# Performance work log

Measured on AMD Instinct MI355X. Metric: run time of the kernel, lower is better.

Reference implementation:

```python
import jax, jax.numpy as jnp
import numpy as np

HEADS = 16
NEG_INF = np.float32(-2**32 + 1)  # matches TF code's padding value


def setup_inputs() -> dict:
    key = jax.random.key(0)
    ks = jax.random.split(key, 11)
    B, S, D = 2, 2048, 1024
    mk = lambda k, shape: jax.random.normal(k, shape, dtype=jnp.float32)
    return {
        "query": mk(ks[0], (B, S, D)),
        "key":   mk(ks[1], (B, S, D)),
        "value": mk(ks[2], (B, S, D)),
        "Wq": mk(ks[3], (D, D)) * (1.0 / np.sqrt(D)), "bq": jnp.zeros((D,), jnp.float32),
        "Wk": mk(ks[4], (D, D)) * (1.0 / np.sqrt(D)), "bk": jnp.zeros((D,), jnp.float32),
        "Wv": mk(ks[5], (D, D)) * (1.0 / np.sqrt(D)), "bv": jnp.zeros((D,), jnp.float32),
        "Wo": mk(ks[6], (D, D)) * (1.0 / np.sqrt(D)), "bo": jnp.zeros((D,), jnp.float32),
    }


def reference(query, key, value, Wq, bq, Wk, bk, Wv, bv, Wo, bo):
    B, S, D = query.shape
    H = HEADS
    dh = D // H
    # QKV projections with relu (as in the original Dense(activation=relu))
    q = jax.nn.relu(query @ Wq + bq).reshape(B, S, H, dh)
    k = jax.nn.relu(key   @ Wk + bk).reshape(B, S, H, dh)
    v = jax.nn.relu(value @ Wv + bv).reshape(B, S, H, dh)
    # scaled dot-product attention; scale = sqrt(per-head key dim)
    scores = jnp.einsum("bqhd,bkhd->bhqk", q, k) / jnp.sqrt(jnp.float32(dh))
    # causal mask (masked=True path): zeros above the diagonal -> NEG_INF
    causal = jnp.tril(jnp.ones((S, S), dtype=jnp.float32))  # [S,S]
    scores = jnp.where(causal == 0, NEG_INF, scores)
    attn = jax.nn.softmax(scores, axis=-1)  # [B,H,S,S]
    out = jnp.einsum("bhqk,bkhd->bqhd", attn, v).reshape(B, S, D)
    return jax.nn.relu(out @ Wo + bo)
```

## Files before the change

### kernel.cpp

```cpp
#include <hip/hip_runtime.h>
#include <hip/hip_bf16.h>

using bf16 = __hip_bfloat16;
typedef __attribute__((ext_vector_type(8))) short bf16x8;
typedef __attribute__((ext_vector_type(4))) float f32x4;

#define DEV __device__ __forceinline__

DEV void gload_lds16(const void* g, void* l) {
  __builtin_amdgcn_global_load_lds((const __attribute__((address_space(1))) void*)g,
                                   (__attribute__((address_space(3))) void*)l, 16, 0, 0);
}

DEV unsigned pk2(float lo, float hi) {
  union { bf16 h[2]; unsigned u; } z;
  z.h[0] = __float2bfloat16(lo);
  z.h[1] = __float2bfloat16(hi);
  return z.u;
}

struct PrepArgs {
  const float* x[3]; bf16* y[3];
  const float* W[4]; bf16* WT[4];
};

__global__ __launch_bounds__(256) void prep_kernel(PrepArgs a) {
  __shared__ float tile[32][33];
  const int b = blockIdx.x;
  if (b < 6144) {
    const int which = b >> 11, blk = b & 2047;
    const int i = blk * 256 + threadIdx.x;
    const float4* xv = (const float4*)a.x[which];
    float4 p = xv[i * 2];
    float4 q = xv[i * 2 + 1];
    union { bf16 h[8]; uint4 v; } u;
    u.h[0] = __float2bfloat16(p.x); u.h[1] = __float2bfloat16(p.y);
    u.h[2] = __float2bfloat16(p.z); u.h[3] = __float2bfloat16(p.w);
    u.h[4] = __float2bfloat16(q.x); u.h[5] = __float2bfloat16(q.y);
    u.h[6] = __float2bfloat16(q.z); u.h[7] = __float2bfloat16(q.w);
    *(uint4*)&a.y[which][(size_t)i * 8] = u.v;
  } else {
    const int w = (b - 6144) >> 10, blk = (b - 6144) & 1023;
    const float* W = a.W[w];
    bf16* WT = a.WT[w];
    const int tx = threadIdx.x & 31, ty = threadIdx.x >> 5;
    const int n0 = (blk & 31) * 32, k0 = (blk >> 5) * 32;
#pragma unroll
    for (int i = ty; i < 32; i += 8)
      tile[i][tx] = W[(size_t)(k0 + i) * 1024 + n0 + tx];
    __syncthreads();
#pragma unroll
    for (int i = ty; i < 32; i += 8)
      WT[(size_t)(n0 + i) * 1024 + k0 + tx] = __float2bfloat16(tile[tx][i]);
  }
}

__global__ __launch_bounds__(256) void vtrans_kernel(const bf16* __restrict__ v,
                                                     bf16* __restrict__ VT) {
  __shared__ bf16 tile[64 * 64];
  const int t = threadIdx.x;
  const int bh = blockIdx.y, b = bh >> 4, h = bh & 15;
  const int s0 = blockIdx.x * 64;
  const int r0 = t >> 3, c8 = t & 7;
#pragma unroll
  for (int it = 0; it < 2; ++it) {
    int r = it * 32 + r0;
    uint4 d = *(const uint4*)&v[(size_t)(b * 2048 + s0 + r) * 1024 + h * 64 + c8 * 8];
    *(uint4*)&tile[r * 64 + ((c8 ^ (r >> 3)) * 8)] = d;
  }
  __syncthreads();
#pragma unroll
  for (int it = 0; it < 2; ++it) {
    int d = it * 32 + r0;
    int sc = c8 * 8;
    union { bf16 h[8]; uint4 v4; } u;
#pragma unroll
    for (int j = 0; j < 8; ++j) {
      int row = sc + j;
      u.h[j] = tile[row * 64 + (((d >> 3) ^ (row >> 3)) * 8) + (d & 7)];
    }
    *(uint4*)&VT[((size_t)bh * 64 + d) * 2048 + s0 + sc] = u.v4;
  }
}

template <typename OutT>
DEV void gemm128_core(const bf16* __restrict__ A, const bf16* __restrict__ BT,
                      const float* __restrict__ bias, OutT* __restrict__ out) {
  constexpr int K = 1024, N = 1024;
  __shared__ bf16 ldsA[2][128 * 32];
  __shared__ bf16 ldsB[2][128 * 32];
  const int t = threadIdx.x;
  const int lane = t & 63, wid = t >> 6;
  const int wr = wid >> 1, wc = wid & 1;
  const int fr = lane & 15, fko = (lane >> 4) * 8;
  const size_t mBase = (size_t)blockIdx.y * 128;
  const size_t nBase = (size_t)blockIdx.x * 128;

  const int srow = t >> 2;
  const int scol = (t & 3) * 8;
  const bf16* gA = A + (mBase + srow) * K + scol;
  const bf16* gB = BT + (nBase + srow) * K + scol;
  const int ldst = wid * 512;

  f32x4 acc[4][4];
#pragma unroll
  for (int i = 0; i < 4; ++i)
#pragma unroll
    for (int j = 0; j < 4; ++j) acc[i][j] = (f32x4){0.f, 0.f, 0.f, 0.f};

  gload_lds16(gA, &ldsA[0][ldst]);
  gload_lds16(gA + 64 * K, &ldsA[0][ldst + 2048]);
  gload_lds16(gB, &ldsB[0][ldst]);
  gload_lds16(gB + 64 * K, &ldsB[0][ldst + 2048]);
  __syncthreads();

  int buf = 0;
  for (int k0 = 0; k0 < K; k0 += 32) {
    if (k0 + 32 < K) {
      const int kn = k0 + 32;
      gload_lds16(gA + kn, &ldsA[buf ^ 1][ldst]);
      gload_lds16(gA + 64 * K + kn, &ldsA[buf ^ 1][ldst + 2048]);
      gload_lds16(gB + kn, &ldsB[buf ^ 1][ldst]);
      gload_lds16(gB + 64 * K + kn, &ldsB[buf ^ 1][ldst + 2048]);
    }
    bf16x8 aF[4], bF[4];
#pragma unroll
    for (int i = 0; i < 4; ++i)
      aF[i] = *(const bf16x8*)&ldsA[buf][(wr * 64 + i * 16 + fr) * 32 + fko];
#pragma unroll
    for (int j = 0; j < 4; ++j)
      bF[j] = *(const bf16x8*)&ldsB[buf][(wc * 64 + j * 16 + fr) * 32 + fko];
#pragma unroll
    for (int i = 0; i < 4; ++i)
#pragma unroll
      for (int j = 0; j < 4; ++j)
        acc[i][j] = __builtin_amdgcn_mfma_f32_16x16x32_bf16(aF[i], bF[j], acc[i][j], 0, 0, 0);
    __syncthreads();
    buf ^= 1;
  }

  const int orow = (int)mBase + wr * 64 + (lane >> 4) * 4;
  const int ocol = (int)nBase + wc * 64 + fr;
#pragma unroll
  for (int j = 0; j < 4; ++j) {
    const float bj = bias[ocol + j * 16];
#pragma unroll
    for (int i = 0; i < 4; ++i)
#pragma unroll
      for (int r = 0; r < 4; ++r) {
        float v = fmaxf(acc[i][j][r] + bj, 0.f);
        size_t idx = (size_t)(orow + i * 16 + r) * N + (ocol + j * 16);
        if constexpr (sizeof(OutT) == 2) out[idx] = __float2bfloat16(v);
        else out[idx] = v;
      }
  }
}

struct QKVArgs {
  const bf16* A[3];
  const bf16* BT[3];
  const float* bias[3];
  bf16* out[3];
};

__global__ __launch_bounds__(256) void gemm_qkv_kernel(QKVArgs args) {
  const int z = blockIdx.z;
  gemm128_core<bf16>(args.A[z], args.BT[z], args.bias[z], args.out[z]);
}

__global__ __launch_bounds__(256) void gemm_out_kernel(const bf16* __restrict__ A,
                                                       const bf16* __restrict__ BT,
                                                       const float* __restrict__ bias,
                                                       float* __restrict__ out) {
  gemm128_core<float>(A, BT, bias, out);
}

__global__ __launch_bounds__(256, 4) void attn_kernel(const bf16* __restrict__ Qb,
                                                      const bf16* __restrict__ Kb,
                                                      const bf16* __restrict__ VTb,
                                                      bf16* __restrict__ Ob) {
  constexpr int Dm = 1024, S = 2048;
  __shared__ bf16 ldsKV[16384];
  const int t = threadIdx.x, l = t & 63, wid = t >> 6;

  const int lin = blockIdx.y * 16 + blockIdx.x;
  const int swz = (lin & 7) * 64 + (lin >> 3);
  const int bh = swz >> 4, pairp = swz & 15;
  const int b = bh >> 4, h = bh & 15;
  const int q4 = l & 15, fg = l >> 4;
  const bf16* Qg = Qb + (size_t)b * S * Dm + h * 64;
  const bf16* Kg = Kb + (size_t)b * S * Dm + h * 64;
  const bf16* VTg = VTb + (size_t)bh * 64 * S;

  const int srow = l >> 3;
  const int schunk = (l & 7) ^ srow;
  const bf16* kSrc = Kg + (size_t)(wid * 16 + srow) * Dm + schunk * 8;
  const bf16* vSrc = VTg + (size_t)(wid * 16 + srow) * S + schunk * 8;
  bf16* kDst = ldsKV + wid * 1024;
  bf16* vDst = ldsKV + 8192 + wid * 1024;

  const int idx0 = ((q4 + ((l & 16) ? 32 : 0)) << 2);
  const int idx1 = idx0 + 64;

#pragma unroll 1
  for (int ph = 0; ph < 2; ++ph) {
    const int qt = ph ? (31 - pairp) : pairp;
    const int qb = qt * 64;
    const int qw = qb + wid * 16;

    bf16x8 qF[2];
#pragma unroll
    for (int kd = 0; kd < 2; ++kd)
      qF[kd] = *(const bf16x8*)&Qg[(size_t)(qw + q4) * Dm + kd * 32 + fg * 8];

    f32x4 oacc[4];
#pragma unroll
    for (int n = 0; n < 4; ++n) oacc[n] = (f32x4){0.f, 0.f, 0.f, 0.f};
    float mrow = -3.0e38f, lsum = 0.f;

    const int nTiles = qt + 1;

    gload_lds16(kSrc, kDst);
    gload_lds16(kSrc + 8 * Dm, kDst + 512);
    gload_lds16(vSrc, vDst);
    gload_lds16(vSrc + 8 * S, vDst + 512);
    __syncthreads();

    int buf = 0;
    for (int tile = 0; tile < nTiles; ++tile) {
      const int kvb = tile * 64;
      if (tile + 1 < nTiles) {
        const int nb = kvb + 64;
        gload_lds16(kSrc + (size_t)nb * Dm, kDst + (buf ^ 1) * 4096);
        gload_lds16(kSrc + (size_t)(nb + 8) * Dm, kDst + (buf ^ 1) * 4096 + 512);
        gload_lds16(vSrc + nb, vDst + (buf ^ 1) * 4096);
        gload_lds16(vSrc + nb + 8 * S, vDst + (buf ^ 1) * 4096 + 512);
      }
      const bf16* kb = ldsKV + buf * 4096;
      const bf16* vb = ldsKV + 8192 + buf * 4096;

      f32x4 sT[4];
#pragma unroll
      for (int n = 0; n < 4; ++n) sT[n] = (f32x4){0.f, 0.f, 0.f, 0.f};
      __builtin_amdgcn_s_setprio(1);
#pragma unroll
      for (int n = 0; n < 4; ++n) {
#pragma unroll
        for (int kd = 0; kd < 2; ++kd) {
          bf16x8 kf = *(const bf16x8*)&kb[(n * 16 + q4) * 64 + (((kd * 4 + fg) ^ (q4 & 7)) * 8)];
          sT[n] = __builtin_amdgcn_mfma_f32_16x16x32_bf16(kf, qF[kd], sT[n], 0, 0, 0);
        }
      }
      __builtin_amdgcn_s_setprio(0);
      const bool needmask = (tile == nTiles - 1);
      const int qrow = qw + q4;
#pragma unroll
      for (int n = 0; n < 4; ++n)
#pragma unroll
        for (int r = 0; r < 4; ++r) {
          float vv = sT[n][r] * 0.125f;
          if (needmask) {
            int kv = kvb + n * 16 + fg * 4 + r;
            if (kv > qrow) vv = -1e30f;
          }
          sT[n][r] = vv;
        }
      float tmax = -3.0e38f;
#pragma unroll
      for (int n = 0; n < 4; ++n)
        tmax = fmaxf(tmax, fmaxf(fmaxf(sT[n][0], sT[n][1]), fmaxf(sT[n][2], sT[n][3])));
      tmax = fmaxf(tmax, __shfl_xor(tmax, 16, 64));
      tmax = fmaxf(tmax, __shfl_xor(tmax, 32, 64));
      const float mnew = fmaxf(mrow, tmax);
      const float corr = __expf(mrow - mnew);
      mrow = mnew;
      float rs = 0.f;
#pragma unroll
      for (int n = 0; n < 4; ++n)
#pragma unroll
        for (int r = 0; r < 4; ++r) {
          float p = __expf(sT[n][r] - mnew);
          sT[n][r] = p;
          rs += p;
        }
      rs += __shfl_xor(rs, 16, 64);
      rs += __shfl_xor(rs, 32, 64);
      lsum = lsum * corr + rs;
#pragma unroll
      for (int n = 0; n < 4; ++n)
#pragma unroll
        for (int r = 0; r < 4; ++r) oacc[n][r] *= corr;

#pragma unroll
      for (int ks = 0; ks < 2; ++ks) {
        const unsigned X0 = pk2(sT[2 * ks][0], sT[2 * ks][1]);
        const unsigned X1 = pk2(sT[2 * ks][2], sT[2 * ks][3]);
        const unsigned Y0 = pk2(sT[2 * ks + 1][0], sT[2 * ks + 1][1]);
        const unsigned Y1 = pk2(sT[2 * ks + 1][2], sT[2 * ks + 1][3]);
        union { int u[4]; bf16x8 v; } bfr;
        {
          int zx = __builtin_amdgcn_ds_bpermute(idx0, (int)X0);
          int zy = __builtin_amdgcn_ds_bpermute(idx0, (int)Y0);
          bfr.u[0] = (l & 32) ? zy : zx;
          zx = __builtin_amdgcn_ds_bpermute(idx0, (int)X1);
          zy = __builtin_amdgcn_ds_bpermute(idx0, (int)Y1);
          bfr.u[1] = (l & 32) ? zy : zx;
          zx = __builtin_amdgcn_ds_bpermute(idx1, (int)X0);
          zy = __builtin_amdgcn_ds_bpermute(idx1, (int)Y0);
          bfr.u[2] = (l & 32) ? zy : zx;
          zx = __builtin_amdgcn_ds_bpermute(idx1, (int)X1);
          zy = __builtin_amdgcn_ds_bpermute(idx1, (int)Y1);
          bfr.u[3] = (l & 32) ? zy : zx;
        }
        __builtin_amdgcn_s_setprio(1);
#pragma unroll
        for (int dblk = 0; dblk < 4; ++dblk) {
          bf16x8 vf = *(const bf16x8*)&vb[(dblk * 16 + q4) * 64 + (((ks * 4 + fg) ^ (q4 & 7)) * 8)];
          oacc[dblk] = __builtin_amdgcn_mfma_f32_16x16x32_bf16(vf, bfr.v, oacc[dblk], 0, 0, 0);
        }
        __builtin_amdgcn_s_setprio(0);
      }
      __syncthreads();
      buf ^= 1;
    }

    bf16* ldsT = ldsKV + wid * 1152;
    const float inv = 1.f / lsum;
#pragma unroll
    for (int dblk = 0; dblk < 4; ++dblk)
#pragma unroll
      for (int r = 0; r < 4; ++r) {
        int d = dblk * 16 + fg * 4 + r;
        ldsT[q4 * 72 + d] = __float2bfloat16(oacc[dblk][r] * inv);
      }
    asm volatile("s_waitcnt lgkmcnt(0)" ::: "memory");
    __builtin_amdgcn_sched_barrier(0);
    const int rq = l >> 2, dq = (l & 3) * 16;
#pragma unroll
    for (int i = 0; i < 2; ++i) {
      uint4 w = *(const uint4*)&ldsT[rq * 72 + dq + 8 * i];
      *(uint4*)&Ob[((size_t)b * S + qw + rq) * Dm + h * 64 + dq + 8 * i] = w;
    }
    __syncthreads();
  }
}

extern "C" void kernel_launch(void* const* d_in, const int* in_sizes, int n_in,
                              void* d_out, int out_size, void* d_ws, size_t ws_size,
                              hipStream_t stream) {
  const float* query = (const float*)d_in[0];
  const float* key   = (const float*)d_in[1];
  const float* value = (const float*)d_in[2];
  const float* Wq = (const float*)d_in[3]; const float* bq = (const float*)d_in[4];
  const float* Wk = (const float*)d_in[5]; const float* bk = (const float*)d_in[6];
  const float* Wv = (const float*)d_in[7]; const float* bv = (const float*)d_in[8];
  const float* Wo = (const float*)d_in[9]; const float* bo = (const float*)d_in[10];
  float* out = (float*)d_out;

  char* ws = (char*)d_ws;
  const size_t MB = 1024 * 1024;
  bf16* xq  = (bf16*)(ws + 0 * MB);
  bf16* xk  = (bf16*)(ws + 8 * MB);
  bf16* xv  = (bf16*)(ws + 16 * MB);
  bf16* qp  = (bf16*)(ws + 24 * MB);
  bf16* kp  = (bf16*)(ws + 32 * MB);
  bf16* vp  = (bf16*)(ws + 40 * MB);
  bf16* WqT = (bf16*)(ws + 48 * MB);
  bf16* WkT = (bf16*)(ws + 50 * MB);
  bf16* WvT = (bf16*)(ws + 52 * MB);
  bf16* WoT = (bf16*)(ws + 54 * MB);
  bf16* VT   = xq;
  bf16* attn = xk;

  PrepArgs pa;
  pa.x[0] = query; pa.x[1] = key; pa.x[2] = value;
  pa.y[0] = xq; pa.y[1] = xk; pa.y[2] = xv;
  pa.W[0] = Wq; pa.W[1] = Wk; pa.W[2] = Wv; pa.W[3] = Wo;
  pa.WT[0] = WqT; pa.WT[1] = WkT; pa.WT[2] = WvT; pa.WT[3] = WoT;
  prep_kernel<<<10240, 256, 0, stream>>>(pa);

  QKVArgs qa;
  qa.A[0] = xq;  qa.A[1] = xk;  qa.A[2] = xv;
  qa.BT[0] = WqT; qa.BT[1] = WkT; qa.BT[2] = WvT;
  qa.bias[0] = bq; qa.bias[1] = bk; qa.bias[2] = bv;
  qa.out[0] = qp; qa.out[1] = kp; qa.out[2] = vp;
  gemm_qkv_kernel<<<dim3(8, 32, 3), 256, 0, stream>>>(qa);

  vtrans_kernel<<<dim3(32, 32), 256, 0, stream>>>(vp, VT);
  attn_kernel<<<dim3(16, 32), 256, 0, stream>>>(qp, kp, VT, attn);
  gemm_out_kernel<<<dim3(8, 32), 256, 0, stream>>>(attn, WoT, bo, out);
}
```

Measured before the change: 233.7 us.

## Use exp2 softmax with lazy rescale and smaller output GEMM tiles

The attention softmax now folds log2(e) into the score scale and uses the hardware exp2 instruction. The running-max rescale of the accumulators is skipped unless some row's max grows by more than 8 (in log2 units). This cuts exp and multiply work per tile, at the cost of intermediate values that can reach up to 2^8 before bf16 packing. Separately, the output projection GEMM uses 64-row tiles with twice as many blocks to fill the GPU better, and both GEMM kernels get launch_bounds occupancy hints.

```diff
diff --git a/kernel.cpp b/kernel.cpp
--- a/kernel.cpp
+++ b/kernel.cpp
@@ -6,6 +6,8 @@
 typedef __attribute__((ext_vector_type(4))) float f32x4;
 
 #define DEV __device__ __forceinline__
+
+DEV float exp2fast(float x) { return __builtin_amdgcn_exp2f(x); }
 
 DEV void gload_lds16(const void* g, void* l) {
   __builtin_amdgcn_global_load_lds((const __attribute__((address_space(1))) void*)g,
@@ -83,17 +85,18 @@
   }
 }
 
-template <typename OutT>
-DEV void gemm128_core(const bf16* __restrict__ A, const bf16* __restrict__ BT,
-                      const float* __restrict__ bias, OutT* __restrict__ out) {
+template <int BM, typename OutT>
+DEV void gemm_core(const bf16* __restrict__ A, const bf16* __restrict__ BT,
+                   const float* __restrict__ bias, OutT* __restrict__ out) {
   constexpr int K = 1024, N = 1024;
-  __shared__ bf16 ldsA[2][128 * 32];
+  constexpr int MI = BM / 32;
+  __shared__ bf16 ldsA[2][BM * 32];
   __shared__ bf16 ldsB[2][128 * 32];
   const int t = threadIdx.x;
   const int lane = t & 63, wid = t >> 6;
   const int wr = wid >> 1, wc = wid & 1;
   const int fr = lane & 15, fko = (lane >> 4) * 8;
-  const size_t mBase = (size_t)blockIdx.y * 128;
+  const size_t mBase = (size_t)blockIdx.y * BM;
   const size_t nBase = (size_t)blockIdx.x * 128;
 
   const int srow = t >> 2;
@@ -102,14 +105,14 @@
   const bf16* gB = BT + (nBase + srow) * K + scol;
   const int ldst = wid * 512;
 
-  f32x4 acc[4][4];
-#pragma unroll
-  for (int i = 0; i < 4; ++i)
+  f32x4 acc[MI][4];
+#pragma unroll
+  for (int i = 0; i < MI; ++i)
 #pragma unroll
     for (int j = 0; j < 4; ++j) acc[i][j] = (f32x4){0.f, 0.f, 0.f, 0.f};
 
   gload_lds16(gA, &ldsA[0][ldst]);
-  gload_lds16(gA + 64 * K, &ldsA[0][ldst + 2048]);
+  if constexpr (BM == 128) gload_lds16(gA + 64 * K, &ldsA[0][ldst + 2048]);
   gload_lds16(gB, &ldsB[0][ldst]);
   gload_lds16(gB + 64 * K, &ldsB[0][ldst + 2048]);
   __syncthreads();
@@ -119,19 +122,19 @@
     if (k0 + 32 < K) {
       const int kn = k0 + 32;
       gload_lds16(gA + kn, &ldsA[buf ^ 1][ldst]);
-      gload_lds16(gA + 64 * K + kn, &ldsA[buf ^ 1][ldst + 2048]);
+      if constexpr (BM == 128) gload_lds16(gA + 64 * K + kn, &ldsA[buf ^ 1][ldst + 2048]);
       gload_lds16(gB + kn, &ldsB[buf ^ 1][ldst]);
       gload_lds16(gB + 64 * K + kn, &ldsB[buf ^ 1][ldst + 2048]);
     }
-    bf16x8 aF[4], bF[4];
-#pragma unroll
-    for (int i = 0; i < 4; ++i)
-      aF[i] = *(const bf16x8*)&ldsA[buf][(wr * 64 + i * 16 + fr) * 32 + fko];
+    bf16x8 aF[MI], bF[4];
+#pragma unroll
+    for (int i = 0; i < MI; ++i)
+      aF[i] = *(const bf16x8*)&ldsA[buf][(wr * (BM / 2) + i * 16 + fr) * 32 + fko];
 #pragma unroll
     for (int j = 0; j < 4; ++j)
       bF[j] = *(const bf16x8*)&ldsB[buf][(wc * 64 + j * 16 + fr) * 32 + fko];
 #pragma unroll
-    for (int i = 0; i < 4; ++i)
+    for (int i = 0; i < MI; ++i)
 #pragma unroll
       for (int j = 0; j < 4; ++j)
         acc[i][j] = __builtin_amdgcn_mfma_f32_16x16x32_bf16(aF[i], bF[j], acc[i][j], 0, 0, 0);
@@ -139,13 +142,13 @@
     buf ^= 1;
   }
 
-  const int orow = (int)mBase + wr * 64 + (lane >> 4) * 4;
+  const int orow = (int)mBase + wr * (BM / 2) + (lane >> 4) * 4;
   const int ocol = (int)nBase + wc * 64 + fr;
 #pragma unroll
   for (int j = 0; j < 4; ++j) {
     const float bj = bias[ocol + j * 16];
 #pragma unroll
-    for (int i = 0; i < 4; ++i)
+    for (int i = 0; i < MI; ++i)
 #pragma unroll
       for (int r = 0; r < 4; ++r) {
         float v = fmaxf(acc[i][j][r] + bj, 0.f);
@@ -163,16 +166,16 @@
   bf16* out[3];
 };
 
-__global__ __launch_bounds__(256) void gemm_qkv_kernel(QKVArgs args) {
+__global__ __launch_bounds__(256, 4) void gemm_qkv_kernel(QKVArgs args) {
   const int z = blockIdx.z;
-  gemm128_core<bf16>(args.A[z], args.BT[z], args.bias[z], args.out[z]);
-}
-
-__global__ __launch_bounds__(256) void gemm_out_kernel(const bf16* __restrict__ A,
-                                                       const bf16* __restrict__ BT,
-                                                       const float* __restrict__ bias,
-                                                       float* __restrict__ out) {
-  gemm128_core<float>(A, BT, bias, out);
+  gemm_core<128, bf16>(args.A[z], args.BT[z], args.bias[z], args.out[z]);
+}
+
+__global__ __launch_bounds__(256, 4) void gemm_out_kernel(const bf16* __restrict__ A,
+                                                          const bf16* __restrict__ BT,
+                                                          const float* __restrict__ bias,
+                                                          float* __restrict__ out) {
+  gemm_core<64, float>(A, BT, bias, out);
 }
 
 __global__ __launch_bounds__(256, 4) void attn_kernel(const bf16* __restrict__ Qb,
@@ -201,6 +204,7 @@
 
   const int idx0 = ((q4 + ((l & 16) ? 32 : 0)) << 2);
   const int idx1 = idx0 + 64;
+  constexpr float SC = 0.18033688f;
 
 #pragma unroll 1
   for (int ph = 0; ph < 2; ++ph) {
@@ -258,38 +262,41 @@
       for (int n = 0; n < 4; ++n)
 #pragma unroll
         for (int r = 0; r < 4; ++r) {
-          float vv = sT[n][r] * 0.125f;
+          float vv = sT[n][r] * SC;
           if (needmask) {
             int kv = kvb + n * 16 + fg * 4 + r;
             if (kv > qrow) vv = -1e30f;
           }
           sT[n][r] = vv;
         }
-      float tmax = -3.0e38f;
+      float vm[4];
 #pragma unroll
       for (int n = 0; n < 4; ++n)
-        tmax = fmaxf(tmax, fmaxf(fmaxf(sT[n][0], sT[n][1]), fmaxf(sT[n][2], sT[n][3])));
+        vm[n] = fmaxf(fmaxf(sT[n][0], sT[n][1]), fmaxf(sT[n][2], sT[n][3]));
+      float tmax = fmaxf(fmaxf(vm[0], vm[1]), fmaxf(vm[2], vm[3]));
       tmax = fmaxf(tmax, __shfl_xor(tmax, 16, 64));
       tmax = fmaxf(tmax, __shfl_xor(tmax, 32, 64));
-      const float mnew = fmaxf(mrow, tmax);
-      const float corr = __expf(mrow - mnew);
-      mrow = mnew;
-      float rs = 0.f;
-#pragma unroll
-      for (int n = 0; n < 4; ++n)
-#pragma unroll
-        for (int r = 0; r < 4; ++r) {
-          float p = __expf(sT[n][r] - mnew);
-          sT[n][r] = p;
-          rs += p;
-        }
+      if (__any(tmax > mrow + 8.f)) {
+        const float mnew = fmaxf(mrow, tmax);
+        const float corr = exp2fast(mrow - mnew);
+        mrow = mnew;
+        lsum *= corr;
+#pragma unroll
+        for (int n = 0; n < 4; ++n)
+#pragma unroll
+          for (int r = 0; r < 4; ++r) oacc[n][r] *= corr;
+      }
+      float rv[4];
+#pragma unroll
+      for (int n = 0; n < 4; ++n) {
+#pragma unroll
+        for (int r = 0; r < 4; ++r) sT[n][r] = exp2fast(sT[n][r] - mrow);
+        rv[n] = (sT[n][0] + sT[n][1]) + (sT[n][2] + sT[n][3]);
+      }
+      float rs = (rv[0] + rv[1]) + (rv[2] + rv[3]);
       rs += __shfl_xor(rs, 16, 64);
       rs += __shfl_xor(rs, 32, 64);
-      lsum = lsum * corr + rs;
-#pragma unroll
-      for (int n = 0; n < 4; ++n)
-#pragma unroll
-        for (int r = 0; r < 4; ++r) oacc[n][r] *= corr;
+      lsum += rs;
 
 #pragma unroll
       for (int ks = 0; ks < 2; ++ks) {
@@ -298,20 +305,19 @@
         const unsigned Y0 = pk2(sT[2 * ks + 1][0], sT[2 * ks + 1][1]);
         const unsigned Y1 = pk2(sT[2 * ks + 1][2], sT[2 * ks + 1][3]);
         union { int u[4]; bf16x8 v; } bfr;
-        {
-          int zx = __builtin_amdgcn_ds_bpermute(idx0, (int)X0);
-          int zy = __builtin_amdgcn_ds_bpermute(idx0, (int)Y0);
-          bfr.u[0] = (l & 32) ? zy : zx;
-          zx = __builtin_amdgcn_ds_bpermute(idx0, (int)X1);
-          zy = __builtin_amdgcn_ds_bpermute(idx0, (int)Y1);
-          bfr.u[1] = (l & 32) ? zy : zx;
-          zx = __builtin_amdgcn_ds_bpermute(idx1, (int)X0);
-          zy = __builtin_amdgcn_ds_bpermute(idx1, (int)Y0);
-          bfr.u[2] = (l & 32) ? zy : zx;
-          zx = __builtin_amdgcn_ds_bpermute(idx1, (int)X1);
-          zy = __builtin_amdgcn_ds_bpermute(idx1, (int)Y1);
-          bfr.u[3] = (l & 32) ? zy : zx;
-        }
+        int zx, zy;
+        zx = __builtin_amdgcn_ds_bpermute(idx0, (int)X0);
+        zy = __builtin_amdgcn_ds_bpermute(idx0, (int)Y0);
+        bfr.u[0] = (l & 32) ? zy : zx;
+        zx = __builtin_amdgcn_ds_bpermute(idx0, (int)X1);
+        zy = __builtin_amdgcn_ds_bpermute(idx0, (int)Y1);
+        bfr.u[1] = (l & 32) ? zy : zx;
+        zx = __builtin_amdgcn_ds_bpermute(idx1, (int)X0);
+        zy = __builtin_amdgcn_ds_bpermute(idx1, (int)Y0);
+        bfr.u[2] = (l & 32) ? zy : zx;
+        zx = __builtin_amdgcn_ds_bpermute(idx1, (int)X1);
+        zy = __builtin_amdgcn_ds_bpermute(idx1, (int)Y1);
+        bfr.u[3] = (l & 32) ? zy : zx;
         __builtin_amdgcn_s_setprio(1);
 #pragma unroll
         for (int dblk = 0; dblk < 4; ++dblk) {
@@ -388,5 +394,5 @@
 
   vtrans_kernel<<<dim3(32, 32), 256, 0, stream>>>(vp, VT);
   attn_kernel<<<dim3(16, 32), 256, 0, stream>>>(qp, kp, VT, attn);
-  gemm_out_kernel<<<dim3(8, 32), 256, 0, stream>>>(attn, WoT, bo, out);
-}
+  gemm_out_kernel<<<dim3(8, 64), 256, 0, stream>>>(attn, WoT, bo, out);
+}
```

Measured after the change: 233.3 us. No clear change (-0.2%).
